# Kernel tuning notes

Hardware: AMD Instinct MI355X
Metric: run time of the kernel (lower is better)

The kernel has to match this reference:

```python
import jax, jax.numpy as jnp
import numpy as np

N_NODES = 10000
IN_CH = 128
OUT_CH = 128
N_EDGES = 320000


def setup_inputs() -> dict:
    key = jax.random.key(0)
    k1, k2, k3, k4 = jax.random.split(key, 4)
    x = jax.random.normal(k1, (N_NODES, IN_CH), dtype=jnp.float32)
    edge_index = jax.random.randint(k2, (N_EDGES, 2), 0, N_NODES, dtype=jnp.int64)
    # Linear weights (torch stores [out, in]); scale like kaiming-uniform-ish
    w = jax.random.normal(k3, (OUT_CH, IN_CH), dtype=jnp.float32) / np.sqrt(IN_CH)
    b = jax.random.normal(k4, (OUT_CH, IN_CH), dtype=jnp.float32) / np.sqrt(IN_CH)
    return {"x": x, "edge_index": edge_index, "w": w, "b": b}


def reference(x, edge_index, w, b):
    n = x.shape[0]
    # Each edge (i, j) contributes x[j] to node i and x[i] to node j (undirected).
    src = jnp.concatenate([edge_index[:, 1], edge_index[:, 0]])  # feature source
    dst = jnp.concatenate([edge_index[:, 0], edge_index[:, 1]])  # aggregation target
    # segment-sum of gathered neighbor features -> [n, in_ch]
    agg_sum = jax.ops.segment_sum(x[src], dst, num_segments=n)
    deg = jax.ops.segment_sum(jnp.ones_like(dst, dtype=x.dtype), dst, num_segments=n)
    # mean with zero fallback for isolated nodes (original uses zeros vector)
    agg = jnp.where(deg[:, None] > 0, agg_sum / jnp.maximum(deg, 1.0)[:, None], 0.0)
    # out = ReLU(agg @ w^T + x @ b^T)
    return jax.nn.relu(agg @ w.T + x @ b.T)
```

## Files before the change

### kernel.cpp

```cpp
#include <hip/hip_runtime.h>

#define N_NODES 10000
#define CH 128
#define N_EDGES 320000
#define CAP 128
#define CSTR 16

#define FILL_BLOCKS ((N_EDGES + 255) / 256)
#define CONV_THREADS (N_NODES * CH / 8)
#define CONV_BLOCKS ((CONV_THREADS + 255) / 256)
#define NPB 16


__device__ __forceinline__ unsigned short f2bf(float f) {
    unsigned u = __float_as_uint(f);
    return (unsigned short)((u + 0x7FFFu + ((u >> 16) & 1u)) >> 16);
}
__device__ __forceinline__ float bf2f(unsigned short h) {
    return __uint_as_float(((unsigned)h) << 16);
}

__global__ __launch_bounds__(256) void fill_conv_kernel(const int* __restrict__ ei,
                                                        int* __restrict__ cursor,
                                                        unsigned short* __restrict__ adj,
                                                        const float* __restrict__ x,
                                                        unsigned short* __restrict__ xb)
{
    const int bid = blockIdx.x;
    if (bid < FILL_BLOCKS) {
        const int t = bid * 256 + threadIdx.x;
        if (t >= N_EDGES) return;
        const int2 p = ((const int2*)ei)[t];
        if ((unsigned)p.x >= N_NODES || (unsigned)p.y >= N_NODES) return;
        const int s0 = atomicAdd(&cursor[p.x * CSTR], 1);
        const int s1 = atomicAdd(&cursor[p.y * CSTR], 1);
        if (s0 < CAP) adj[(size_t)p.x * CAP + s0] = (unsigned short)p.y;
        if (s1 < CAP) adj[(size_t)p.y * CAP + s1] = (unsigned short)p.x;
    } else {
        const int t = (bid - FILL_BLOCKS) * 256 + threadIdx.x;
        if (t >= CONV_THREADS) return;
        const float4 a = ((const float4*)x)[t * 2];
        const float4 c = ((const float4*)x)[t * 2 + 1];
        ushort4 o0, o1;
        o0.x = f2bf(a.x); o0.y = f2bf(a.y); o0.z = f2bf(a.z); o0.w = f2bf(a.w);
        o1.x = f2bf(c.x); o1.y = f2bf(c.y); o1.z = f2bf(c.z); o1.w = f2bf(c.w);
        ((ushort4*)xb)[t * 2]     = o0;
        ((ushort4*)xb)[t * 2 + 1] = o1;
    }
}

__global__ __launch_bounds__(256) void gather_gemm_kernel(const float* __restrict__ x,
                                                          const unsigned short* __restrict__ xb,
                                                          const int* __restrict__ cursor,
                                                          const unsigned short* __restrict__ adj,
                                                          const float* __restrict__ w,
                                                          const float* __restrict__ b,
                                                          float* __restrict__ out)
{
    __shared__ float sh_a[NPB * CH];
    __shared__ float sh_x[NPB * CH];
    const int tid   = threadIdx.x;
    const int node0 = blockIdx.x * NPB;

    const float4 xr0 = ((const float4*)(x + (size_t)node0 * CH))[tid];
    const float4 xr1 = ((const float4*)(x + (size_t)node0 * CH))[tid + 256];

    const int wv   = tid >> 6;
    const int lane = tid & 63;
    const int h    = lane >> 5;
    const int l    = lane & 31;

    for (int i = 0; i < 4; ++i) {
        const int nl   = wv * 4 + i;
        const int node = node0 + nl;
        const int deg  = cursor[node * CSTR];
        const int d    = deg < CAP ? deg : CAP;
        const unsigned short* nb = adj + (size_t)node * CAP;

        float4 acc = {0.f, 0.f, 0.f, 0.f};
        const int nit = (d + 1) >> 1;
#pragma unroll 4
        for (int it = 0; it < nit; ++it) {
            const int idx = 2 * it + h;
            int j = nb[idx];
            j = j < N_NODES ? j : 0;
            const ushort4 u = ((const ushort4*)(xb + (size_t)j * CH))[l];
            const float m = idx < d ? 1.0f : 0.0f;
            acc.x += m * bf2f(u.x);
            acc.y += m * bf2f(u.y);
            acc.z += m * bf2f(u.z);
            acc.w += m * bf2f(u.w);
        }
        acc.x += __shfl_xor(acc.x, 32, 64);
        acc.y += __shfl_xor(acc.y, 32, 64);
        acc.z += __shfl_xor(acc.z, 32, 64);
        acc.w += __shfl_xor(acc.w, 32, 64);

        if (h == 0) {
            const float inv = deg > 0 ? 1.0f / (float)deg : 0.0f;
            float4 o;
            o.x = acc.x * inv; o.y = acc.y * inv;
            o.z = acc.z * inv; o.w = acc.w * inv;
            ((float4*)(sh_a + (size_t)nl * CH))[l] = o;
        }
    }

    ((float4*)sh_x)[tid]       = xr0;
    ((float4*)sh_x)[tid + 256] = xr1;
    __syncthreads();

    const int o = tid & 127;
    const int g = tid >> 7;
    const float4* wr = (const float4*)(w + (size_t)o * CH);
    const float4* br = (const float4*)(b + (size_t)o * CH);
    const float4* A  = (const float4*)(sh_a + (size_t)(g * 8) * CH);
    const float4* X  = (const float4*)(sh_x + (size_t)(g * 8) * CH);

    float acc[8] = {0.f, 0.f, 0.f, 0.f, 0.f, 0.f, 0.f, 0.f};
#pragma unroll 4
    for (int k = 0; k < CH / 4; ++k) {
        const float4 wv4 = wr[k];
        const float4 bv4 = br[k];
#pragma unroll
        for (int n = 0; n < 8; ++n) {
            const float4 a4 = A[n * (CH / 4) + k];
            const float4 x4 = X[n * (CH / 4) + k];
            acc[n] += a4.x * wv4.x + a4.y * wv4.y + a4.z * wv4.z + a4.w * wv4.w
                    + x4.x * bv4.x + x4.y * bv4.y + x4.z * bv4.z + x4.w * bv4.w;
        }
    }
#pragma unroll
    for (int n = 0; n < 8; ++n) {
        const int node = node0 + g * 8 + n;
        const float v = acc[n];
        out[(size_t)node * CH + o] = v > 0.f ? v : 0.f;
    }
}

extern "C" void kernel_launch(void* const* d_in, const int* in_sizes, int n_in,
                              void* d_out, int out_size, void* d_ws, size_t ws_size,
                              hipStream_t stream)
{
    const float* x  = (const float*)d_in[0];
    const int*   ei = (const int*)d_in[1];
    const float* w  = (const float*)d_in[2];
    const float* b  = (const float*)d_in[3];
    float*       out = (float*)d_out;

    int*            cursor = (int*)d_ws;
    unsigned short* adj    = (unsigned short*)((char*)d_ws + 640000);
    unsigned short* xb16   = (unsigned short*)((char*)d_ws + 3200000);

    hipMemsetAsync(d_ws, 0, (size_t)N_NODES * CSTR * sizeof(int), stream);

    fill_conv_kernel<<<FILL_BLOCKS + CONV_BLOCKS, 256, 0, stream>>>(ei, cursor, adj, x, xb16);
    gather_gemm_kernel<<<N_NODES / NPB, 256, 0, stream>>>(x, xb16, cursor, adj, w, b, out);
}
```

Measured before the change: 142.2 us.

## Halve nodes per block and gather 16-byte bf16 rows across four lanes groups

Each gather wave now processes four neighbors at a time, with 16 lanes each loading a 16-byte uint4 of bf16 per neighbor, and reduces across lanes with two xor shuffles. Nodes per block drop from 16 to 8, doubling the grid size to improve load balance and occupancy. The cost is that the w and b rows are re-read by twice as many blocks in the GEMM phase, and there are more shuffle operations per node.

```diff
diff --git a/kernel.cpp b/kernel.cpp
--- a/kernel.cpp
+++ b/kernel.cpp
@@ -9,15 +9,12 @@
 #define FILL_BLOCKS ((N_EDGES + 255) / 256)
 #define CONV_THREADS (N_NODES * CH / 8)
 #define CONV_BLOCKS ((CONV_THREADS + 255) / 256)
-#define NPB 16
+#define NPB 8
 
 
 __device__ __forceinline__ unsigned short f2bf(float f) {
     unsigned u = __float_as_uint(f);
     return (unsigned short)((u + 0x7FFFu + ((u >> 16) & 1u)) >> 16);
-}
-__device__ __forceinline__ float bf2f(unsigned short h) {
-    return __uint_as_float(((unsigned)h) << 16);
 }
 
 __global__ __launch_bounds__(256) void fill_conv_kernel(const int* __restrict__ ei,
@@ -62,67 +59,85 @@
     const int tid   = threadIdx.x;
     const int node0 = blockIdx.x * NPB;
 
-    const float4 xr0 = ((const float4*)(x + (size_t)node0 * CH))[tid];
-    const float4 xr1 = ((const float4*)(x + (size_t)node0 * CH))[tid + 256];
+    const float4 xr = ((const float4*)(x + (size_t)node0 * CH))[tid];
 
     const int wv   = tid >> 6;
     const int lane = tid & 63;
-    const int h    = lane >> 5;
-    const int l    = lane & 31;
+    const int h    = lane >> 4;
+    const int l    = lane & 15;
 
-    for (int i = 0; i < 4; ++i) {
-        const int nl   = wv * 4 + i;
+    for (int i = 0; i < 2; ++i) {
+        const int nl   = wv * 2 + i;
         const int node = node0 + nl;
         const int deg  = cursor[node * CSTR];
         const int d    = deg < CAP ? deg : CAP;
         const unsigned short* nb = adj + (size_t)node * CAP;
 
-        float4 acc = {0.f, 0.f, 0.f, 0.f};
-        const int nit = (d + 1) >> 1;
+        float4 accA = {0.f, 0.f, 0.f, 0.f};
+        float4 accB = {0.f, 0.f, 0.f, 0.f};
+        const int nit = (d + 3) >> 2;
 #pragma unroll 4
         for (int it = 0; it < nit; ++it) {
-            const int idx = 2 * it + h;
+            const int idx = 4 * it + h;
             int j = nb[idx];
             j = j < N_NODES ? j : 0;
-            const ushort4 u = ((const ushort4*)(xb + (size_t)j * CH))[l];
+            const uint4 q = ((const uint4*)(xb + (size_t)j * CH))[l];
             const float m = idx < d ? 1.0f : 0.0f;
-            acc.x += m * bf2f(u.x);
-            acc.y += m * bf2f(u.y);
-            acc.z += m * bf2f(u.z);
-            acc.w += m * bf2f(u.w);
+            accA.x += m * __uint_as_float(q.x << 16);
+            accA.y += m * __uint_as_float(q.x & 0xffff0000u);
+            accA.z += m * __uint_as_float(q.y << 16);
+            accA.w += m * __uint_as_float(q.y & 0xffff0000u);
+            accB.x += m * __uint_as_float(q.z << 16);
+            accB.y += m * __uint_as_float(q.z & 0xffff0000u);
+            accB.z += m * __uint_as_float(q.w << 16);
+            accB.w += m * __uint_as_float(q.w & 0xffff0000u);
         }
-        acc.x += __shfl_xor(acc.x, 32, 64);
-        acc.y += __shfl_xor(acc.y, 32, 64);
-        acc.z += __shfl_xor(acc.z, 32, 64);
-        acc.w += __shfl_xor(acc.w, 32, 64);
+        accA.x += __shfl_xor(accA.x, 16, 64);
+        accA.y += __shfl_xor(accA.y, 16, 64);
+        accA.z += __shfl_xor(accA.z, 16, 64);
+        accA.w += __shfl_xor(accA.w, 16, 64);
+        accB.x += __shfl_xor(accB.x, 16, 64);
+        accB.y += __shfl_xor(accB.y, 16, 64);
+        accB.z += __shfl_xor(accB.z, 16, 64);
+        accB.w += __shfl_xor(accB.w, 16, 64);
+        accA.x += __shfl_xor(accA.x, 32, 64);
+        accA.y += __shfl_xor(accA.y, 32, 64);
+        accA.z += __shfl_xor(accA.z, 32, 64);
+        accA.w += __shfl_xor(accA.w, 32, 64);
+        accB.x += __shfl_xor(accB.x, 32, 64);
+        accB.y += __shfl_xor(accB.y, 32, 64);
+        accB.z += __shfl_xor(accB.z, 32, 64);
+        accB.w += __shfl_xor(accB.w, 32, 64);
 
         if (h == 0) {
             const float inv = deg > 0 ? 1.0f / (float)deg : 0.0f;
-            float4 o;
-            o.x = acc.x * inv; o.y = acc.y * inv;
-            o.z = acc.z * inv; o.w = acc.w * inv;
-            ((float4*)(sh_a + (size_t)nl * CH))[l] = o;
+            float4 o0, o1;
+            o0.x = accA.x * inv; o0.y = accA.y * inv;
+            o0.z = accA.z * inv; o0.w = accA.w * inv;
+            o1.x = accB.x * inv; o1.y = accB.y * inv;
+            o1.z = accB.z * inv; o1.w = accB.w * inv;
+            ((float4*)(sh_a + (size_t)nl * CH))[2 * l]     = o0;
+            ((float4*)(sh_a + (size_t)nl * CH))[2 * l + 1] = o1;
         }
     }
 
-    ((float4*)sh_x)[tid]       = xr0;
-    ((float4*)sh_x)[tid + 256] = xr1;
+    ((float4*)sh_x)[tid] = xr;
     __syncthreads();
 
     const int o = tid & 127;
     const int g = tid >> 7;
     const float4* wr = (const float4*)(w + (size_t)o * CH);
     const float4* br = (const float4*)(b + (size_t)o * CH);
-    const float4* A  = (const float4*)(sh_a + (size_t)(g * 8) * CH);
-    const float4* X  = (const float4*)(sh_x + (size_t)(g * 8) * CH);
+    const float4* A  = (const float4*)(sh_a + (size_t)(g * 4) * CH);
+    const float4* X  = (const float4*)(sh_x + (size_t)(g * 4) * CH);
 
-    float acc[8] = {0.f, 0.f, 0.f, 0.f, 0.f, 0.f, 0.f, 0.f};
+    float acc[4] = {0.f, 0.f, 0.f, 0.f};
 #pragma unroll 4
     for (int k = 0; k < CH / 4; ++k) {
         const float4 wv4 = wr[k];
         const float4 bv4 = br[k];
 #pragma unroll
-        for (int n = 0; n < 8; ++n) {
+        for (int n = 0; n < 4; ++n) {
             const float4 a4 = A[n * (CH / 4) + k];
             const float4 x4 = X[n * (CH / 4) + k];
             acc[n] += a4.x * wv4.x + a4.y * wv4.y + a4.z * wv4.z + a4.w * wv4.w
@@ -130,8 +145,8 @@
         }
     }
 #pragma unroll
-    for (int n = 0; n < 8; ++n) {
-        const int node = node0 + g * 8 + n;
+    for (int n = 0; n < 4; ++n) {
+        const int node = node0 + g * 4 + n;
         const float v = acc[n];
         out[(size_t)node * CH + o] = v > 0.f ? v : 0.f;
     }
```

New measurement: 153.2 us. +7.7%, slower.
